# Kernel optimization log

Hardware: AMD Instinct MI355X
Metric: run time of the kernel (lower is better)

The kernel has to match this reference:

```python
import math
import jax, jax.numpy as jnp
import numpy as np


def _scharr(img):
    # img: (..., H, W) -> (..., 2, H, W); F.conv2d is cross-correlation, as is lax.conv
    kx = jnp.array([[-3., 0., 3.], [10., 0., 10.], [-3., 0., 3.]], jnp.float32)
    k = jnp.stack([kx, kx.T])[:, None]  # (2,1,3,3)
    lead = img.shape[:-2]
    x = img.reshape((-1, 1) + img.shape[-2:])
    y = jax.lax.conv_general_dilated(x, k, (1, 1), 'SAME',
                                     dimension_numbers=('NCHW', 'OIHW', 'NCHW'))
    return y.reshape(lead + (2,) + img.shape[-2:])


def _rotate_nearest(x, angle_deg):
    # torchvision-style rotate with expand=True, nearest interpolation, zero fill
    H, W = x.shape[-2], x.shape[-1]
    a = math.radians(angle_deg)
    c, s = math.cos(a), math.sin(a)
    Hn = int(math.ceil(abs(W * s) + abs(H * c)))
    Wn = int(math.ceil(abs(W * c) + abs(H * s)))
    yy, xx = jnp.meshgrid(jnp.arange(Hn, dtype=jnp.float32),
                          jnp.arange(Wn, dtype=jnp.float32), indexing='ij')
    xg = xx - (Wn - 1) / 2.0
    yg = yy - (Hn - 1) / 2.0
    xi = c * xg - s * yg + (W - 1) / 2.0
    yi = s * xg + c * yg + (H - 1) / 2.0
    xn = jnp.round(xi).astype(jnp.int32)
    yn = jnp.round(yi).astype(jnp.int32)
    valid = (xn >= 0) & (xn < W) & (yn >= 0) & (yn < H)
    out = x[..., jnp.clip(yn, 0, H - 1), jnp.clip(xn, 0, W - 1)]
    return jnp.where(valid, out, jnp.zeros((), x.dtype))


def _gauss_derivs(img):
    # image_gaussian_derivatives: (B, C, H, W) -> (B, C, 8, H, W)
    H, W = img.shape[-2:]
    g = _scharr(img)  # (B, C, 2, H, W)
    # rotated_xywh(H, W, 45) to get crop offsets, exactly as in the source
    a = math.radians(45.0)
    al, be = math.cos(a), math.sin(a)
    cx, cy = W / 2.0, H / 2.0
    pts = [(0., 0.), (W - 1., 0.), (0., H - 1.), (W - 1., H - 1.)]
    rx = [al * px + be * py + (1 - al) * cx - be * cy for px, py in pts]
    ry = [-be * px + al * py + be * cx + (1 - al) * cy for px, py in pts]
    w45 = max(rx) - min(rx)
    h45 = max(ry) - min(ry)
    startx = int(max(0, (w45 - W) / 2))
    starty = int(max(0, (h45 - H) / 2))
    gr = _scharr(_rotate_nearest(img, 45.0))      # (B, C, 2, Hr, Wr)
    grb = _rotate_nearest(gr, -45.0)
    grc = grb[..., starty:starty + H, startx:startx + W]  # (B, C, 2, H, W)
    return jnp.concatenate([jnp.clip(g, 0, None), jnp.clip(g, None, 0),
                            jnp.clip(grc, 0, None), jnp.clip(grc, None, 0)], axis=-3)


def _normalize_min_max(x):
    hmin = x.min(axis=(-2, -1), keepdims=True)
    hmax = x.max(axis=(-2, -1), keepdims=True)
    return (x - hmin) / (hmax - hmin)


def _batched_hist(Z, nbins):
    # Z: (..., N) int in [0, nbins) -> per-row histogram (..., nbins) via one fused segment_sum
    lead = Z.shape[:-1]
    L = int(np.prod(lead))
    Zf = Z.reshape(L, -1)
    ids = (jnp.arange(L, dtype=jnp.int32)[:, None] * nbins + Zf).ravel()
    h = jax.ops.segment_sum(jnp.ones(ids.shape, jnp.float32), ids, num_segments=L * nbins)
    return h.reshape(lead + (nbins,))


def setup_inputs() -> dict:
    key = jax.random.key(0)
    k1, k2 = jax.random.split(key)
    img = jax.random.uniform(k1, (2, 3, 512, 512), jnp.float32)
    reg_lab = jax.random.randint(k2, (2, 1, 3, 512, 512), 0, 256, dtype=jnp.int32)
    return {'img': img, 'reg_lab': reg_lab,
            'color_bins': 25, 'texture_bins': 10, 'num_segments': 256}


def reference(img, reg_lab, color_bins, texture_bins, num_segments):
    B, I, G, H, W = reg_lab.shape
    C = img.shape[1]
    S = num_segments
    # normalized oriented gradient features (B, C, 8, H, W)
    tex = _normalize_min_max(_gauss_derivs(img))
    # region sizes: scatter_add of ones over region labels
    region_sizes = _batched_hist(reg_lab.reshape(B, I, G, H * W), S)  # (B,I,G,S)
    # color histograms
    Zc = (reg_lab[:, :, :, None].astype(jnp.float32) * color_bins
          + img[:, None, None] * (color_bins - 1)).astype(jnp.int32)  # (B,I,G,C,H,W)
    ch = _batched_hist(Zc.reshape(B, I, G, C, H * W), S * color_bins)
    ch = jnp.moveaxis(ch.reshape(B, I, G, C, S, color_bins), -2, -3)  # (B,I,G,S,C,cb)
    ch = ch / ch.sum(axis=(-2, -1), keepdims=True)
    # texture histograms
    Zt = (reg_lab[:, :, :, None, None].astype(jnp.float32) * texture_bins
          + tex[:, None, None] * (texture_bins - 1)).astype(jnp.int32)  # (B,I,G,C,8,H,W)
    th = _batched_hist(Zt.reshape(B, I, G, C, 8, H * W), S * texture_bins)
    th = jnp.moveaxis(th.reshape(B, I, G, C, 8, S, texture_bins), -2, -4)  # (B,I,G,S,C,8,tb)
    th = th / th.sum(axis=(-3, -2, -1), keepdims=True)
    # per-region bounding boxes via segment min/max (replaces the 5-deep python loop)
    grid_y, grid_x = jnp.meshgrid(jnp.arange(H, dtype=jnp.int32),
                                  jnp.arange(W, dtype=jnp.int32), indexing='ij')
    BIG = B * I * G
    ids = (jnp.arange(BIG, dtype=jnp.int32)[:, None] * S
           + reg_lab.reshape(BIG, H * W)).ravel()
    xs = jnp.tile(grid_x.ravel(), BIG)
    ys = jnp.tile(grid_y.ravel(), BIG)
    n = BIG * S
    xmin = jax.ops.segment_min(xs, ids, num_segments=n)
    xmax = jax.ops.segment_max(xs, ids, num_segments=n)
    ymin = jax.ops.segment_min(ys, ids, num_segments=n)
    ymax = jax.ops.segment_max(ys, ids, num_segments=n)
    nonempty = region_sizes.reshape(n) > 0
    xmin = jnp.where(nonempty, xmin, W)
    ymin = jnp.where(nonempty, ymin, H)
    xmax = jnp.where(nonempty, xmax, 0)
    ymax = jnp.where(nonempty, ymax, 0)
    xywh = jnp.stack([xmin, ymin, xmax - xmin, ymax - ymin], axis=-1).reshape(B, I, G, S, 4)
    return region_sizes, ch, th, xywh
```

## Files before the change

kernel.cpp:

```cpp
#include <hip/hip_runtime.h>
#include <climits>

#define HW 262144
#define IW 512
#define RN 725
#define NSEG 256
#define CH_OFF 1536
#define TH_OFF 116736
#define XY_OFF 485376
#define NBLK 256
#define THP 24
#define CHP 32

#define ASTR 67
#define RSTR 73
#define ROFF 156

static __device__ __forceinline__ float rtap_l(const float* __restrict__ Rt,
                                               int rx0, int ry0, int cx, int cy) {
    if (cx < 0 || cx >= RN || cy < 0 || cy >= RN) return 0.f;
    const float cs = 0.7071067811865476f;
    float xg = (float)cx - 362.0f;
    float yg = (float)cy - 362.0f;
    float xi = cs * xg - cs * yg + 255.5f;
    float yi = cs * xg + cs * yg + 255.5f;
    int xs = (int)rintf(xi);
    int ys = (int)rintf(yi);
    if (xs < 0 || xs >= IW || ys < 0 || ys >= IW) return 0.f;
    return Rt[(ys - ry0) * RSTR + (xs - rx0)];
}

static __device__ __forceinline__ void mm_of_map(const float* __restrict__ pmin,
                                                 const float* __restrict__ pmax,
                                                 int m, float* slo, float* shi,
                                                 float& mn, float& mx) {
    int tid = threadIdx.x;
    float lo = 3.4e38f, hi = -3.4e38f;
    for (int i = tid; i < NBLK; i += 256) {
        lo = fminf(lo, pmin[m * NBLK + i]);
        hi = fmaxf(hi, pmax[m * NBLK + i]);
    }
    slo[tid] = lo; shi[tid] = hi;
    __syncthreads();
    for (int off = 128; off > 0; off >>= 1) {
        if (tid < off) {
            slo[tid] = fminf(slo[tid], slo[tid + off]);
            shi[tid] = fmaxf(shi[tid], shi[tid + off]);
        }
        __syncthreads();
    }
    mn = slo[0]; mx = shi[0];
    __syncthreads();
}

__global__ __launch_bounds__(256) void k_front(
    const float* __restrict__ img, const int* __restrict__ lab,
    float* __restrict__ gmaps, float* __restrict__ pmin, float* __restrict__ pmax,
    unsigned char* __restrict__ lab8, unsigned* __restrict__ chp_w,
    unsigned* __restrict__ rsp, int* __restrict__ bxmin, int* __restrict__ bxmax,
    int* __restrict__ bymin, int* __restrict__ bymax)
{
    __shared__ __align__(16) unsigned char smem[20480];
    int bxid = blockIdx.x;
    int tid = threadIdx.x;
    int grp = bxid / 11, rem = bxid % 11;
    if (rem < 8) {
        int u = grp * 8 + rem;
        int tile = u & 255;
        int bc = u >> 8;
        float* At = (float*)smem;
        float* Rt = At + 18 * ASTR;
        float (*slo)[256] = (float (*)[256])(Rt + 24 * RSTR);
        float (*shi)[256] = slo + 4;
        {
            int i = tile * 256 + tid;
            int4 l = ((const int4*)(lab + (size_t)bc * HW))[i];
            unsigned v = (unsigned)(l.x & 255) | ((unsigned)(l.y & 255) << 8) |
                         ((unsigned)(l.z & 255) << 16) | ((unsigned)(l.w & 255) << 24);
            ((unsigned*)(lab8 + (size_t)bc * HW))[i] = v;
        }
        int tx0 = (tile & 7) << 6;
        int ty0 = (tile >> 3) << 4;
        const float* im = img + (size_t)bc * HW;
        int lane = tid & 63, wr = tid >> 6;
        for (int r = wr; r < 18; r += 4) {
            int gy = ty0 - 1 + r;
            bool yok = (gy >= 0 && gy < IW);
            int gx = tx0 - 1 + lane;
            At[r * ASTR + lane] = (yok && gx >= 0 && gx < IW) ? im[gy * IW + gx] : 0.f;
            if (lane < 2) {
                int gx2 = gx + 64;
                At[r * ASTR + lane + 64] = (yok && gx2 >= 0 && gx2 < IW) ? im[gy * IW + gx2] : 0.f;
            }
        }
        for (int r = wr; r < 24; r += 4) {
            int gy = ty0 - ROFF + r;
            bool yok = (gy >= 0 && gy < IW);
            int gx = tx0 - ROFF + lane;
            Rt[r * RSTR + lane] = (yok && gx >= 0 && gx < IW) ? im[gy * IW + gx] : 0.f;
            if (lane < 8) {
                int gx2 = gx + 64;
                Rt[r * RSTR + lane + 64] = (yok && gx2 >= 0 && gx2 < IW) ? im[gy * IW + gx2] : 0.f;
            }
        }
        __syncthreads();
        const float cs = 0.7071067811865476f;
        int rx0 = tx0 - ROFF, ry0 = ty0 - ROFF;
        float mn0 = 3.4e38f, mx0 = -3.4e38f, mn1 = 3.4e38f, mx1 = -3.4e38f;
        float mn2 = 3.4e38f, mx2 = -3.4e38f, mn3 = 3.4e38f, mx3 = -3.4e38f;
        #pragma unroll
        for (int it = 0; it < 4; ++it) {
            int ly = wr * 4 + it;
            int x = tx0 + lane, y = ty0 + ly;
            int p = y * IW + x;
            const float* Ar = At + ly * ASTR + lane;
            float a  = Ar[0],            b2 = Ar[1],            c2 = Ar[2];
            float d2 = Ar[ASTR],                                 e2 = Ar[ASTR + 2];
            float f2 = Ar[2 * ASTR],     h2 = Ar[2 * ASTR + 1], i9 = Ar[2 * ASTR + 2];
            float g0 = -3.f*a + 3.f*c2 + 10.f*d2 + 10.f*e2 - 3.f*f2 + 3.f*i9;
            float g1 = -3.f*a + 10.f*b2 - 3.f*c2 + 3.f*f2 + 10.f*h2 + 3.f*i9;
            gmaps[((size_t)(bc*2+0))*HW + p] = g0;
            gmaps[((size_t)(bc*2+1))*HW + p] = g1;
            float xgc = (float)(x + 105) - 512.5f;
            float ygc = (float)(y + 105) - 512.5f;
            float t1 = cs * xgc, t2 = cs * ygc;
            float xi = (t1 + t2) + 362.0f;
            float yi = (-t1 + t2) + 362.0f;
            int xn = (int)rintf(xi);
            int yn = (int)rintf(yi);
            float r0 = 0.f, r1 = 0.f;
            if (xn >= 0 && xn < RN && yn >= 0 && yn < RN) {
                float ra = rtap_l(Rt, rx0, ry0, xn-1, yn-1);
                float rb = rtap_l(Rt, rx0, ry0, xn,   yn-1);
                float rc = rtap_l(Rt, rx0, ry0, xn+1, yn-1);
                float rd = rtap_l(Rt, rx0, ry0, xn-1, yn);
                float re = rtap_l(Rt, rx0, ry0, xn+1, yn);
                float rf = rtap_l(Rt, rx0, ry0, xn-1, yn+1);
                float rh = rtap_l(Rt, rx0, ry0, xn,   yn+1);
                float ri = rtap_l(Rt, rx0, ry0, xn+1, yn+1);
                r0 = -3.f*ra + 3.f*rc + 10.f*rd + 10.f*re - 3.f*rf + 3.f*ri;
                r1 = -3.f*ra + 10.f*rb - 3.f*rc + 3.f*rf + 10.f*rh + 3.f*ri;
            }
            gmaps[((size_t)(12 + bc*2+0))*HW + p] = r0;
            gmaps[((size_t)(12 + bc*2+1))*HW + p] = r1;
            mn0 = fminf(mn0, g0); mx0 = fmaxf(mx0, g0);
            mn1 = fminf(mn1, g1); mx1 = fmaxf(mx1, g1);
            mn2 = fminf(mn2, r0); mx2 = fmaxf(mx2, r0);
            mn3 = fminf(mn3, r1); mx3 = fmaxf(mx3, r1);
        }
        slo[0][tid] = mn0; shi[0][tid] = mx0;
        slo[1][tid] = mn1; shi[1][tid] = mx1;
        slo[2][tid] = mn2; shi[2][tid] = mx2;
        slo[3][tid] = mn3; shi[3][tid] = mx3;
        __syncthreads();
        for (int off = 128; off > 0; off >>= 1) {
            if (tid < off) {
                #pragma unroll
                for (int k = 0; k < 4; ++k) {
                    slo[k][tid] = fminf(slo[k][tid], slo[k][tid + off]);
                    shi[k][tid] = fmaxf(shi[k][tid], shi[k][tid + off]);
                }
            }
            __syncthreads();
        }
        if (tid < 4) {
            int m = (tid < 2) ? (bc*2 + tid) : (12 + bc*2 + (tid - 2));
            pmin[m * NBLK + tile] = slo[tid][0];
            pmax[m * NBLK + tile] = shi[tid][0];
        }
    } else {
        int w = grp * 3 + (rem - 8);
        int gy = w >> 5;
        int sp = w & 31;
        int c = gy % 3;
        int bg = gy / 3;
        int b = bg / 3;
        unsigned* pk = (unsigned*)smem;
        unsigned* prc = pk + 3200;
        int* sxmin = (int*)(prc + 128);
        int* sxmax = sxmin + NSEG;
        int* symin = sxmax + NSEG;
        int* symax = symin + NSEG;
        bool do_reg = (c == 0);
        for (int i = tid; i < 3200; i += 256) pk[i] = 0;
        if (do_reg) {
            if (tid < 128) prc[tid] = 0;
            sxmin[tid] = INT_MAX; sxmax[tid] = INT_MIN;
            symin[tid] = INT_MAX; symax[tid] = INT_MIN;
        }
        __syncthreads();
        const float4* ip = (const float4*)(img + ((size_t)b * 3 + c) * HW);
        const int4* lp = (const int4*)(lab + (size_t)bg * HW);
        for (int i = sp * 256 + tid; i < HW / 4; i += 256 * CHP) {
            float4 v4 = ip[i];
            int4 l4 = lp[i];
            int l0 = l4.x & 255, l1 = l4.y & 255, l2 = l4.z & 255, l3 = l4.w & 255;
            int b0 = (int)((float)l0 * 25.0f + v4.x * 24.0f);
            int b1 = (int)((float)l1 * 25.0f + v4.y * 24.0f);
            int b2 = (int)((float)l2 * 25.0f + v4.z * 24.0f);
            int b3 = (int)((float)l3 * 25.0f + v4.w * 24.0f);
            b0 = min(max(b0, 0), 6399); b1 = min(max(b1, 0), 6399);
            b2 = min(max(b2, 0), 6399); b3 = min(max(b3, 0), 6399);
            atomicAdd(&pk[b0 >> 1], 1u << ((b0 & 1) << 4));
            atomicAdd(&pk[b1 >> 1], 1u << ((b1 & 1) << 4));
            atomicAdd(&pk[b2 >> 1], 1u << ((b2 & 1) << 4));
            atomicAdd(&pk[b3 >> 1], 1u << ((b3 & 1) << 4));
            if (do_reg) {
                int p = i << 2;
                int y = p >> 9, x = p & 511;
                atomicAdd(&prc[l0 >> 1], 1u << ((l0 & 1) << 4));
                atomicAdd(&prc[l1 >> 1], 1u << ((l1 & 1) << 4));
                atomicAdd(&prc[l2 >> 1], 1u << ((l2 & 1) << 4));
                atomicAdd(&prc[l3 >> 1], 1u << ((l3 & 1) << 4));
                atomicMin(&sxmin[l0], x);     atomicMax(&sxmax[l0], x);
                atomicMin(&sxmin[l1], x + 1); atomicMax(&sxmax[l1], x + 1);
                atomicMin(&sxmin[l2], x + 2); atomicMax(&sxmax[l2], x + 2);
                atomicMin(&sxmin[l3], x + 3); atomicMax(&sxmax[l3], x + 3);
                atomicMin(&symin[l0], y); atomicMax(&symax[l0], y);
                atomicMin(&symin[l1], y); atomicMax(&symax[l1], y);
                atomicMin(&symin[l2], y); atomicMax(&symax[l2], y);
                atomicMin(&symin[l3], y); atomicMax(&symax[l3], y);
            }
        }
        __syncthreads();
        unsigned* dst = chp_w + ((size_t)gy * CHP + sp) * 3200;
        for (int i = tid; i < 3200; i += 256) dst[i] = pk[i];
        if (do_reg) {
            size_t pi = (size_t)(bg * CHP + sp) * NSEG + tid;
            rsp[pi] = (prc[tid >> 1] >> ((tid & 1) << 4)) & 0xFFFFu;
            bxmin[pi] = sxmin[tid]; bxmax[pi] = sxmax[tid];
            bymin[pi] = symin[tid]; bymax[pi] = symax[tid];
        }
    }
}

__global__ __launch_bounds__(256) void k_hist(
    const float* __restrict__ maps, const unsigned char* __restrict__ lab8,
    const float* __restrict__ pmin, const float* __restrict__ pmax,
    unsigned* __restrict__ thp_w, const unsigned* __restrict__ chp_w,
    const unsigned* __restrict__ rsp,
    const int* __restrict__ bxmin, const int* __restrict__ bxmax,
    const int* __restrict__ bymin, const int* __restrict__ bymax,
    float* __restrict__ out)
{
    __shared__ __align__(16) unsigned char smem[22528];
    int bx = blockIdx.x;
    int tid = threadIdx.x;
    if (bx < 1728) {
        unsigned* cnt = (unsigned*)smem;
        float* slo = (float*)(smem + 20480);
        float* shi = slo + 256;
        int gy = bx / THP;
        int split = bx - gy * THP;
        int gi = gy % 3;
        int r = gy / 3;
        int base = r & 1;
        int bd = r >> 1;
        int d = bd & 1;
        int bc = bd >> 1;
        int b = bc / 3;
        int m = base * 12 + bc * 2 + d;
        float mn, mx;
        mm_of_map(pmin, pmax, m, slo, shi, mn, mx);
        for (int i = tid; i < 5120; i += 256) cnt[i] = 0;
        __syncthreads();
        float hminp = fmaxf(mn, 0.f), denp = fmaxf(mx, 0.f) - hminp;
        float hminn = fminf(mn, 0.f), denn = fminf(mx, 0.f) - hminn;
        const float4* src = (const float4*)(maps + (size_t)m * HW);
        const unsigned* lp = (const unsigned*)(lab8 + (size_t)(b * 3 + gi) * HW);
        for (int i = split * 256 + tid; i < HW / 4; i += 256 * THP) {
            float4 v4 = src[i];
            unsigned l4 = lp[i];
#define TH1(V, SH)                                                     \
            {                                                          \
                float v = (V);                                         \
                bool ge = (v >= 0.f);                                  \
                float hm = ge ? hminp : hminn;                         \
                float dn = ge ? denp : denn;                           \
                float t9 = ((v - hm) / dn) * 9.0f;                     \
                int bi = (int)((float)((l4 >> SH) & 255u) * 10.0f + t9); \
                bi = min(max(bi, 0), 2559);                            \
                atomicAdd(&cnt[(ge ? 0 : 2560) + bi], 1u);             \
            }
            TH1(v4.x, 0) TH1(v4.y, 8) TH1(v4.z, 16) TH1(v4.w, 24)
#undef TH1
        }
        __syncthreads();
        unsigned* dst = thp_w + ((size_t)(gy * THP + split)) * 2560;
        for (int i = tid; i < 2560; i += 256)
            dst[i] = cnt[2 * i] | (cnt[2 * i + 1] << 16);
    } else {
        unsigned (*crs)[32] = (unsigned (*)[32])smem;
        int (*sxm)[32] = (int (*)[32])(smem + 256);
        int (*sxM)[32] = (int (*)[32])(smem + 512);
        int (*sym)[32] = (int (*)[32])(smem + 768);
        int (*syM)[32] = (int (*)[32])(smem + 1024);
        int j = bx - 1728;
        int seg0 = j * 2;
        int bg = seg0 >> 8;
        int s0 = seg0 & 255, s1 = s0 + 1;
        int g = tid >> 5, w = tid & 31;
        size_t base0 = (size_t)(bg * CHP + w) * NSEG;
        if (g == 0)      crs[0][w] = rsp[base0 + s0];
        else if (g == 1) sxm[0][w] = bxmin[base0 + s0];
        else if (g == 2) sxM[0][w] = bxmax[base0 + s0];
        else if (g == 3) sym[0][w] = bymin[base0 + s0];
        else if (g == 4) syM[0][w] = bymax[base0 + s0];
        else if (g == 5) crs[1][w] = rsp[base0 + s1];
        else if (g == 6) sxm[1][w] = bxmin[base0 + s1];
        else if (g == 7) sxM[1][w] = bxmax[base0 + s1];
        if (g == 0)      sym[1][w] = bymin[base0 + s1];
        else if (g == 1) syM[1][w] = bymax[base0 + s1];
        __syncthreads();
        int half = tid >> 7, t2 = tid & 127;
        int s = half ? s1 : s0;
        int seg = seg0 + half;
        if (t2 < 75) {
            unsigned rs = 0;
            #pragma unroll 4
            for (int p = 0; p < CHP; ++p) rs += crs[half][p];
            float rsf = (float)rs;
            int c = t2 / 25, cb = t2 - c * 25;
            int bin = s * 25 + cb;
            unsigned sum = 0;
            #pragma unroll 4
            for (int p = 0; p < CHP; ++p) {
                unsigned v = chp_w[((size_t)((bg * 3 + c) * CHP + p)) * 3200 + (bin >> 1)];
                sum += (v >> ((bin & 1) << 4)) & 0xFFFFu;
            }
            out[CH_OFF + (size_t)seg * 75 + t2] = (float)sum / (3.0f * rsf);
        } else if (t2 == 75) {
            unsigned rs = 0;
            #pragma unroll 4
            for (int p = 0; p < CHP; ++p) rs += crs[half][p];
            float rsf = (float)rs;
            out[seg] = rsf;
            int xmn = INT_MAX, xmx = INT_MIN, ymn = INT_MAX, ymx = INT_MIN;
            #pragma unroll 4
            for (int p = 0; p < CHP; ++p) {
                xmn = min(xmn, sxm[half][p]); xmx = max(xmx, sxM[half][p]);
                ymn = min(ymn, sym[half][p]); ymx = max(ymx, syM[half][p]);
            }
            if (!(rsf > 0.f)) { xmn = IW; ymn = IW; xmx = 0; ymx = 0; }
            float* xy = out + XY_OFF + (size_t)seg * 4;
            xy[0] = (float)xmn; xy[1] = (float)ymn;
            xy[2] = (float)(xmx - xmn); xy[3] = (float)(ymx - ymn);
        }
    }
}

__global__ __launch_bounds__(256) void k_final(
    const unsigned* __restrict__ thp_w, const unsigned* __restrict__ rsp,
    const float* __restrict__ pmin, const float* __restrict__ pmax,
    float* __restrict__ out)
{
    __shared__ unsigned hist[640];
    __shared__ unsigned srs[32];
    __shared__ float slo[256], shi[256];
    int tid = threadIdx.x;
    int bx = blockIdx.x;
    int gy = bx >> 3;
    int ck = bx & 7;
    int l0 = ck << 5;
    int gi = gy % 3; int r = gy / 3; int base = r & 1;
    int bd = r >> 1; int d = bd & 1; int bc = bd >> 1;
    int b = bc / 3, c = bc - b * 3;
    int m = base * 12 + bc * 2 + d;
    int bg = b * 3 + gi;
    float mn, mx;
    mm_of_map(pmin, pmax, m, slo, shi, mn, mx);
    for (int w = tid; w < 320; w += 256) {
        int gw = (w < 160) ? (l0 * 5 + w) : (1280 + l0 * 5 + (w - 160));
        unsigned s0 = 0, s1 = 0;
        #pragma unroll 4
        for (int p = 0; p < THP; ++p) {
            unsigned v = thp_w[((size_t)(gy * THP + p)) * 2560 + gw];
            s0 += v & 0xFFFFu; s1 += v >> 16;
        }
        int bi = (w < 160) ? (2 * w) : (320 + 2 * (w - 160));
        hist[bi] = s0; hist[bi + 1] = s1;
    }
    if (tid < 32) {
        unsigned s = 0;
        #pragma unroll 4
        for (int p = 0; p < CHP; ++p) s += rsp[((size_t)(bg * CHP + p)) * NSEG + l0 + tid];
        srs[tid] = s;
    }
    __syncthreads();
    if (tid < 32) {
        int l = l0 + tid;
        unsigned nge = 0;
        for (int tb = 0; tb < 10; ++tb) nge += hist[tid * 10 + tb];
        unsigned rsu = srs[tid];
        unsigned nlt = (rsu >= nge) ? (rsu - nge) : 0u;
        float hminp = fmaxf(mn, 0.f), denp = fmaxf(mx, 0.f) - hminp;
        float hminn = fminf(mn, 0.f), denn = fminf(mx, 0.f) - hminn;
        float la = (float)l;
        float tp0 = ((0.0f - hminp) / denp) * 9.0f;
        float tn0 = ((0.0f - hminn) / denn) * 9.0f;
        int g0off = l0 * 10;
        int bp = (int)(la * 10.0f + tp0); bp = min(max(bp, 0), 2559);
        int bn = (int)(la * 10.0f + tn0); bn = min(max(bn, 0), 2559);
        if (nlt && bp >= g0off && bp < g0off + 320) atomicAdd(&hist[bp - g0off], nlt);
        if (nge && bn >= g0off && bn < g0off + 320) atomicAdd(&hist[320 + bn - g0off], nge);
    }
    __syncthreads();
    for (int i = tid; i < 640; i += 256) {
        int pos = (i < 320);
        int rr = pos ? i : i - 320;
        int lseg = rr / 10, tb = rr % 10;
        int seg = l0 + lseg;
        int tt = base * 4 + (pos ? 0 : 2) + d;
        float rsf = (float)srs[lseg];
        out[TH_OFF + ((size_t)(bg * NSEG + seg) * 3 + c) * 80 + tt * 10 + tb] =
            (float)hist[i] / (24.0f * rsf);
    }
}

extern "C" void kernel_launch(void* const* d_in, const int* in_sizes, int n_in,
                              void* d_out, int out_size, void* d_ws, size_t ws_size,
                              hipStream_t stream) {
    const float* img = (const float*)d_in[0];
    const int* lab = (const int*)d_in[1];
    float* out = (float*)d_out;

    float* gmaps = (float*)d_ws;
    float* pmin = gmaps + (size_t)24 * HW;
    float* pmax = pmin + 24 * NBLK;
    unsigned* thp_w = (unsigned*)(pmax + 24 * NBLK);
    unsigned* chp_w = thp_w + (size_t)72 * THP * 2560;
    unsigned char* lab8 = (unsigned char*)(chp_w + (size_t)18 * CHP * 3200);
    unsigned* rsp = (unsigned*)(lab8 + (size_t)6 * HW);
    int* bxmin = (int*)(rsp + 6 * CHP * NSEG);
    int* bxmax = bxmin + 6 * CHP * NSEG;
    int* bymin = bxmax + 6 * CHP * NSEG;
    int* bymax = bymin + 6 * CHP * NSEG;

    hipLaunchKernelGGL(k_front, dim3(2112), dim3(256), 0, stream,
                       img, lab, gmaps, pmin, pmax, lab8, chp_w, rsp, bxmin, bxmax, bymin, bymax);
    hipLaunchKernelGGL(k_hist, dim3(1728 + 768), dim3(256), 0, stream,
                       gmaps, lab8, pmin, pmax, thp_w, chp_w, rsp, bxmin, bxmax, bymin, bymax, out);
    hipLaunchKernelGGL(k_final, dim3(576), dim3(256), 0, stream,
                       thp_w, rsp, pmin, pmax, out);
}
```

Baseline: 116.2 us.

## Spread region stats across channel blocks and cut texture histogram splits

In the front kernel, the region-size and bounding-box atomics now run in all three channel blocks, each taking every third loop iteration, instead of only the channel-0 block. The per-region partials grow from 32 to 96 slices, and the consumers in k_hist and k_final reduce over 96 partials. k_final does that reduction with all threads in parallel. The texture histogram split drops from 24 to 16 blocks per group, and the region-finalize blocks now handle 4 segments each, so fewer blocks are launched. The aim is to remove the load imbalance in which channel-0 blocks did far more atomic work, at the cost of more partial data to write and reduce.

```diff
diff --git a/kernel.cpp b/kernel.cpp
--- a/kernel.cpp
+++ b/kernel.cpp
@@ -9,7 +9,7 @@
 #define TH_OFF 116736
 #define XY_OFF 485376
 #define NBLK 256
-#define THP 24
+#define THP 16
 #define CHP 32
 
 #define ASTR 67
@@ -181,17 +181,15 @@
         int* sxmax = sxmin + NSEG;
         int* symin = sxmax + NSEG;
         int* symax = symin + NSEG;
-        bool do_reg = (c == 0);
         for (int i = tid; i < 3200; i += 256) pk[i] = 0;
-        if (do_reg) {
-            if (tid < 128) prc[tid] = 0;
-            sxmin[tid] = INT_MAX; sxmax[tid] = INT_MIN;
-            symin[tid] = INT_MAX; symax[tid] = INT_MIN;
-        }
+        if (tid < 128) prc[tid] = 0;
+        sxmin[tid] = INT_MAX; sxmax[tid] = INT_MIN;
+        symin[tid] = INT_MAX; symax[tid] = INT_MIN;
         __syncthreads();
         const float4* ip = (const float4*)(img + ((size_t)b * 3 + c) * HW);
         const int4* lp = (const int4*)(lab + (size_t)bg * HW);
-        for (int i = sp * 256 + tid; i < HW / 4; i += 256 * CHP) {
+        int itc = 0;
+        for (int i = sp * 256 + tid; i < HW / 4; i += 256 * CHP, ++itc) {
             float4 v4 = ip[i];
             int4 l4 = lp[i];
             int l0 = l4.x & 255, l1 = l4.y & 255, l2 = l4.z & 255, l3 = l4.w & 255;
@@ -205,7 +203,7 @@
             atomicAdd(&pk[b1 >> 1], 1u << ((b1 & 1) << 4));
             atomicAdd(&pk[b2 >> 1], 1u << ((b2 & 1) << 4));
             atomicAdd(&pk[b3 >> 1], 1u << ((b3 & 1) << 4));
-            if (do_reg) {
+            if (itc % 3 == c) {
                 int p = i << 2;
                 int y = p >> 9, x = p & 511;
                 atomicAdd(&prc[l0 >> 1], 1u << ((l0 & 1) << 4));
@@ -225,12 +223,10 @@
         __syncthreads();
         unsigned* dst = chp_w + ((size_t)gy * CHP + sp) * 3200;
         for (int i = tid; i < 3200; i += 256) dst[i] = pk[i];
-        if (do_reg) {
-            size_t pi = (size_t)(bg * CHP + sp) * NSEG + tid;
-            rsp[pi] = (prc[tid >> 1] >> ((tid & 1) << 4)) & 0xFFFFu;
-            bxmin[pi] = sxmin[tid]; bxmax[pi] = sxmax[tid];
-            bymin[pi] = symin[tid]; bymax[pi] = symax[tid];
-        }
+        size_t pi = (size_t)((bg * 32 + sp) * 3 + c) * NSEG + tid;
+        rsp[pi] = (prc[tid >> 1] >> ((tid & 1) << 4)) & 0xFFFFu;
+        bxmin[pi] = sxmin[tid]; bxmax[pi] = sxmax[tid];
+        bymin[pi] = symin[tid]; bymax[pi] = symax[tid];
     }
 }
 
@@ -246,12 +242,12 @@
     __shared__ __align__(16) unsigned char smem[22528];
     int bx = blockIdx.x;
     int tid = threadIdx.x;
-    if (bx < 1728) {
+    if (bx < 1152) {
         unsigned* cnt = (unsigned*)smem;
         float* slo = (float*)(smem + 20480);
         float* shi = slo + 256;
-        int gy = bx / THP;
-        int split = bx - gy * THP;
+        int gy = bx >> 4;
+        int split = bx & 15;
         int gi = gy % 3;
         int r = gy / 3;
         int base = r & 1;
@@ -290,61 +286,61 @@
         for (int i = tid; i < 2560; i += 256)
             dst[i] = cnt[2 * i] | (cnt[2 * i + 1] << 16);
     } else {
-        unsigned (*crs)[32] = (unsigned (*)[32])smem;
-        int (*sxm)[32] = (int (*)[32])(smem + 256);
-        int (*sxM)[32] = (int (*)[32])(smem + 512);
-        int (*sym)[32] = (int (*)[32])(smem + 768);
-        int (*syM)[32] = (int (*)[32])(smem + 1024);
-        int j = bx - 1728;
-        int seg0 = j * 2;
+        unsigned* crs2 = (unsigned*)smem;
+        int* xm = (int*)(crs2 + 192);
+        int* xM = xm + 192;
+        int* ym = xM + 192;
+        int* yM = ym + 192;
+        int j = bx - 1152;
+        int seg0 = j * 4;
         int bg = seg0 >> 8;
-        int s0 = seg0 & 255, s1 = s0 + 1;
-        int g = tid >> 5, w = tid & 31;
-        size_t base0 = (size_t)(bg * CHP + w) * NSEG;
-        if (g == 0)      crs[0][w] = rsp[base0 + s0];
-        else if (g == 1) sxm[0][w] = bxmin[base0 + s0];
-        else if (g == 2) sxM[0][w] = bxmax[base0 + s0];
-        else if (g == 3) sym[0][w] = bymin[base0 + s0];
-        else if (g == 4) syM[0][w] = bymax[base0 + s0];
-        else if (g == 5) crs[1][w] = rsp[base0 + s1];
-        else if (g == 6) sxm[1][w] = bxmin[base0 + s1];
-        else if (g == 7) sxM[1][w] = bxmax[base0 + s1];
-        if (g == 0)      sym[1][w] = bymin[base0 + s1];
-        else if (g == 1) syM[1][w] = bymax[base0 + s1];
-        __syncthreads();
-        int half = tid >> 7, t2 = tid & 127;
-        int s = half ? s1 : s0;
-        int seg = seg0 + half;
-        if (t2 < 75) {
-            unsigned rs = 0;
-            #pragma unroll 4
-            for (int p = 0; p < CHP; ++p) rs += crs[half][p];
-            float rsf = (float)rs;
-            int c = t2 / 25, cb = t2 - c * 25;
-            int bin = s * 25 + cb;
-            unsigned sum = 0;
-            #pragma unroll 4
-            for (int p = 0; p < CHP; ++p) {
-                unsigned v = chp_w[((size_t)((bg * 3 + c) * CHP + p)) * 3200 + (bin >> 1)];
-                sum += (v >> ((bin & 1) << 4)) & 0xFFFFu;
-            }
-            out[CH_OFF + (size_t)seg * 75 + t2] = (float)sum / (3.0f * rsf);
-        } else if (t2 == 75) {
-            unsigned rs = 0;
-            #pragma unroll 4
-            for (int p = 0; p < CHP; ++p) rs += crs[half][p];
-            float rsf = (float)rs;
-            out[seg] = rsf;
-            int xmn = INT_MAX, xmx = INT_MIN, ymn = INT_MAX, ymx = INT_MIN;
-            #pragma unroll 4
-            for (int p = 0; p < CHP; ++p) {
-                xmn = min(xmn, sxm[half][p]); xmx = max(xmx, sxM[half][p]);
-                ymn = min(ymn, sym[half][p]); ymx = max(ymx, syM[half][p]);
-            }
-            if (!(rsf > 0.f)) { xmn = IW; ymn = IW; xmx = 0; ymx = 0; }
-            float* xy = out + XY_OFF + (size_t)seg * 4;
-            xy[0] = (float)xmn; xy[1] = (float)ymn;
-            xy[2] = (float)(xmx - xmn); xy[3] = (float)(ymx - ymn);
+        for (int ps = 0; ps < 2; ++ps) {
+            int sb = (seg0 & 255) + ps * 2;
+            for (int k = tid; k < 960; k += 256) {
+                int a = k / 192;
+                int rk = k - a * 192;
+                int h = rk / 96, p = rk - h * 96;
+                size_t idx = ((size_t)(bg * 96 + p)) * NSEG + (sb + h);
+                int o = h * 96 + p;
+                if (a == 0)      crs2[o] = rsp[idx];
+                else if (a == 1) xm[o] = bxmin[idx];
+                else if (a == 2) xM[o] = bxmax[idx];
+                else if (a == 3) ym[o] = bymin[idx];
+                else             yM[o] = bymax[idx];
+            }
+            __syncthreads();
+            int half = tid >> 7, t2 = tid & 127;
+            int s = sb + half;
+            int seg = bg * 256 + s;
+            if (t2 < 75) {
+                unsigned rs = 0;
+                for (int p = 0; p < 96; ++p) rs += crs2[half * 96 + p];
+                float rsf = (float)rs;
+                int cc = t2 / 25, cb = t2 - cc * 25;
+                int bin = s * 25 + cb;
+                unsigned sum = 0;
+                #pragma unroll 4
+                for (int p = 0; p < CHP; ++p) {
+                    unsigned v = chp_w[((size_t)((bg * 3 + cc) * CHP + p)) * 3200 + (bin >> 1)];
+                    sum += (v >> ((bin & 1) << 4)) & 0xFFFFu;
+                }
+                out[CH_OFF + (size_t)seg * 75 + t2] = (float)sum / (3.0f * rsf);
+            } else if (t2 == 75) {
+                unsigned rs = 0;
+                for (int p = 0; p < 96; ++p) rs += crs2[half * 96 + p];
+                float rsf = (float)rs;
+                out[seg] = rsf;
+                int xmn = INT_MAX, xmx = INT_MIN, ymn = INT_MAX, ymx = INT_MIN;
+                for (int p = 0; p < 96; ++p) {
+                    xmn = min(xmn, xm[half * 96 + p]); xmx = max(xmx, xM[half * 96 + p]);
+                    ymn = min(ymn, ym[half * 96 + p]); ymx = max(ymx, yM[half * 96 + p]);
+                }
+                if (!(rsf > 0.f)) { xmn = IW; ymn = IW; xmx = 0; ymx = 0; }
+                float* xy = out + XY_OFF + (size_t)seg * 4;
+                xy[0] = (float)xmn; xy[1] = (float)ymn;
+                xy[2] = (float)(xmx - xmn); xy[3] = (float)(ymx - ymn);
+            }
+            __syncthreads();
         }
     }
 }
@@ -355,6 +351,7 @@
     float* __restrict__ out)
 {
     __shared__ unsigned hist[640];
+    __shared__ unsigned srsp[256];
     __shared__ unsigned srs[32];
     __shared__ float slo[256], shi[256];
     int tid = threadIdx.x;
@@ -380,18 +377,23 @@
         int bi = (w < 160) ? (2 * w) : (320 + 2 * (w - 160));
         hist[bi] = s0; hist[bi + 1] = s1;
     }
+    {
+        int l = tid >> 3, g = tid & 7;
+        unsigned s = 0;
+        for (int p = g * 12; p < g * 12 + 12; ++p)
+            s += rsp[((size_t)(bg * 96 + p)) * NSEG + l0 + l];
+        srsp[tid] = s;
+    }
+    __syncthreads();
     if (tid < 32) {
         unsigned s = 0;
-        #pragma unroll 4
-        for (int p = 0; p < CHP; ++p) s += rsp[((size_t)(bg * CHP + p)) * NSEG + l0 + tid];
+        #pragma unroll
+        for (int g = 0; g < 8; ++g) s += srsp[tid * 8 + g];
         srs[tid] = s;
-    }
-    __syncthreads();
-    if (tid < 32) {
         int l = l0 + tid;
         unsigned nge = 0;
         for (int tb = 0; tb < 10; ++tb) nge += hist[tid * 10 + tb];
-        unsigned rsu = srs[tid];
+        unsigned rsu = s;
         unsigned nlt = (rsu >= nge) ? (rsu - nge) : 0u;
         float hminp = fmaxf(mn, 0.f), denp = fmaxf(mx, 0.f) - hminp;
         float hminn = fminf(mn, 0.f), denn = fminf(mx, 0.f) - hminn;
@@ -431,14 +433,14 @@
     unsigned* chp_w = thp_w + (size_t)72 * THP * 2560;
     unsigned char* lab8 = (unsigned char*)(chp_w + (size_t)18 * CHP * 3200);
     unsigned* rsp = (unsigned*)(lab8 + (size_t)6 * HW);
-    int* bxmin = (int*)(rsp + 6 * CHP * NSEG);
-    int* bxmax = bxmin + 6 * CHP * NSEG;
-    int* bymin = bxmax + 6 * CHP * NSEG;
-    int* bymax = bymin + 6 * CHP * NSEG;
+    int* bxmin = (int*)(rsp + 6 * 96 * NSEG);
+    int* bxmax = bxmin + 6 * 96 * NSEG;
+    int* bymin = bxmax + 6 * 96 * NSEG;
+    int* bymax = bymin + 6 * 96 * NSEG;
 
     hipLaunchKernelGGL(k_front, dim3(2112), dim3(256), 0, stream,
                        img, lab, gmaps, pmin, pmax, lab8, chp_w, rsp, bxmin, bxmax, bymin, bymax);
-    hipLaunchKernelGGL(k_hist, dim3(1728 + 768), dim3(256), 0, stream,
+    hipLaunchKernelGGL(k_hist, dim3(1152 + 384), dim3(256), 0, stream,
                        gmaps, lab8, pmin, pmax, thp_w, chp_w, rsp, bxmin, bxmax, bymin, bymax, out);
     hipLaunchKernelGGL(k_final, dim3(576), dim3(256), 0, stream,
                        thp_w, rsp, pmin, pmax, out);
```

Result: slower. 124.6 us (+7.2%).
